# Optimization experiments

Measured on AMD Instinct MI355X. Metric: run time of the kernel, lower is better.

## Reference

```python
import jax, jax.numpy as jnp
import numpy as np

B, S, E, H = 8, 1024, 1152, 16  # batch, seq, embed_dim, num_heads
D = E // H  # head_dim = 72


def setup_inputs() -> dict:
    k = jax.random.key(0)
    ks = jax.random.split(k, 5)
    s_in = (2.0 / (E + E)) ** 0.5  # xavier-ish scale for packed proj
    return {
        "query": jax.random.normal(ks[0], (B, S, E), jnp.float32),
        "key": jax.random.normal(ks[1], (B, S, E), jnp.float32),
        "value": jax.random.normal(ks[2], (B, S, E), jnp.float32),
        "in_proj_weight": jax.random.normal(ks[3], (E, 3 * E), jnp.float32) * s_in,
        "in_proj_bias": jnp.zeros((3 * E,), jnp.float32),
        "out_w": jax.random.normal(ks[4], (E, E), jnp.float32) * s_in,
        "out_b": jnp.zeros((E,), jnp.float32),
    }


def reference(query, key, value, in_proj_weight, in_proj_bias, out_w, out_b):
    qb_, ss, _ = query.shape
    b, s, _ = value.shape
    qb, kb, vb = jnp.split(in_proj_bias, 3, -1)
    qw, kw, vw = jnp.split(in_proj_weight, 3, -1)
    q = (query @ qw + qb).reshape(qb_, ss, H, D)
    k = (key @ kw + kb).reshape(b, s, H, D)
    v = (value @ vw + vb).reshape(b, s, H, D)
    scale = D ** (-0.5)
    scores = jnp.einsum("bqhd,bkhd->bhqk", q * scale, k)  # [B,H,Sq,Sk]
    attn = jnp.einsum("bhqk,bkhd->bqhd", jax.nn.softmax(scores, axis=-1), v)
    return attn.reshape(qb_, ss, E) @ out_w + out_b
```

## Files before the change

kernel.cpp:

```cpp
#include <hip/hip_runtime.h>
#include <hip/hip_bf16.h>
#include <math.h>
#include <stdint.h>

static constexpr int Bb = 8, S = 1024, E = 1152, H = 16, D = 72;
static constexpr int N3 = 3 * E;
static constexpr long QKV_T = (long)Bb * H * S * D;

typedef __attribute__((ext_vector_type(8))) short bf16x8;
typedef __attribute__((ext_vector_type(4))) short bf16x4;
typedef __attribute__((ext_vector_type(4))) float f32x4;

#define MFMA16(A, B, C) __builtin_amdgcn_mfma_f32_16x16x32_bf16(A, B, C, 0, 0, 0)

__device__ __forceinline__ short f2bf(float f) {
    __hip_bfloat16 h = __float2bfloat16(f);
    return __builtin_bit_cast(short, h);
}
__device__ __forceinline__ unsigned packbf(float lo, float hi) {
    return (unsigned)(unsigned short)f2bf(lo) | ((unsigned)(unsigned short)f2bf(hi) << 16);
}

__device__ __forceinline__ void gload_lds16(const void* g, void* l) {
    __builtin_amdgcn_global_load_lds(
        (const __attribute__((address_space(1))) unsigned int*)g,
        (__attribute__((address_space(3))) unsigned int*)l, 16, 0, 0);
}

__global__ __launch_bounds__(256)
void wt_conv(const float* __restrict__ W, short* __restrict__ WT, int K, int N)
{
    __shared__ float tt[32][33];
    const int n0 = blockIdx.x * 32, k0 = blockIdx.y * 32;
    const int t = threadIdx.x;
    {
        int r = t >> 3, c4 = (t & 7) * 4;
        float4 v = *reinterpret_cast<const float4*>(W + (long)(k0 + r) * N + n0 + c4);
        tt[r][c4 + 0] = v.x; tt[r][c4 + 1] = v.y; tt[r][c4 + 2] = v.z; tt[r][c4 + 3] = v.w;
    }
    __syncthreads();
    {
        int n = t >> 3, k4 = (t & 7) * 4;
        bf16x4 o = {f2bf(tt[k4 + 0][n]), f2bf(tt[k4 + 1][n]),
                    f2bf(tt[k4 + 2][n]), f2bf(tt[k4 + 3][n])};
        *reinterpret_cast<bf16x4*>(WT + (long)(n0 + n) * K + k0 + k4) = o;
    }
}

__global__ __launch_bounds__(256)
void tobf16(const float* __restrict__ X, short* __restrict__ Y, long n4)
{
    for (long i = (long)blockIdx.x * 256 + threadIdx.x; i < n4; i += (long)gridDim.x * 256) {
        float4 v = reinterpret_cast<const float4*>(X)[i];
        bf16x4 o = {f2bf(v.x), f2bf(v.y), f2bf(v.z), f2bf(v.w)};
        reinterpret_cast<bf16x4*>(Y)[i] = o;
    }
}

__global__ __launch_bounds__(256)
void qkv_proj_one(const short* __restrict__ Xb, const short* __restrict__ WTn,
                  const float* __restrict__ bias, short* __restrict__ qkvW, int which)
{
    __shared__ short aT[128][32], bW[128][32];
    const int tid = threadIdx.x, lane = tid & 63, w = tid >> 6;
    const int c = lane & 15, g = lane >> 4;
    const int m0 = blockIdx.x * 128, n0 = blockIdx.y * 128;
    const int wm = (w >> 1) * 64, wn = (w & 1) * 64;
    const int lrow = lane >> 2, lch = (lane & 3) * 8;

    f32x4 acc[4][4] = {};

    for (int k0 = 0; k0 < E; k0 += 32) {
        __syncthreads();
        for (int t = 0; t < 2; ++t) {
            int row = w * 32 + t * 16;
            gload_lds16(Xb + (long)(m0 + row + lrow) * E + k0 + lch, &aT[row][0]);
            gload_lds16(WTn + (long)(n0 + row + lrow) * E + k0 + lch, &bW[row][0]);
        }
        __syncthreads();

        bf16x8 af[4], bh[4];
        for (int i = 0; i < 4; ++i) {
            af[i] = *reinterpret_cast<const bf16x8*>(&aT[wm + i * 16 + c][g * 8]);
            bh[i] = *reinterpret_cast<const bf16x8*>(&bW[wn + i * 16 + c][g * 8]);
        }
        for (int i = 0; i < 4; ++i)
            for (int j = 0; j < 4; ++j)
                acc[i][j] = MFMA16(af[i], bh[j], acc[i][j]);
    }

    for (int j = 0; j < 4; ++j) {
        int n = n0 + wn + j * 16 + c;
        float bv = bias[n];
        int hh = n / D, dd = n % D;
        if (which < 2) {
            for (int i = 0; i < 4; ++i) {
                int rowb = m0 + wm + i * 16 + g * 4;
                for (int r = 0; r < 4; ++r) {
                    int row = rowb + r;
                    int b = row >> 10, s = row & 1023;
                    qkvW[((long)(b * H + hh) * S + s) * D + dd] = f2bf(acc[i][j][r] + bv);
                }
            }
        } else {
            int cx = dd & 7;
            for (int i = 0; i < 4; ++i) {
                int srow = m0 + wm + i * 16 + g * 4;
                int b = srow >> 10, s = srow & 1023;
                int sw = (s & ~63) | ((((s >> 3) & 7) ^ cx) << 3) | (s & 7);
                bf16x4 pk = {f2bf(acc[i][j][0] + bv), f2bf(acc[i][j][1] + bv),
                             f2bf(acc[i][j][2] + bv), f2bf(acc[i][j][3] + bv)};
                *reinterpret_cast<bf16x4*>(&qkvW[((long)(b * H + hh) * D + dd) * S + sw]) = pk;
            }
        }
    }
}

__global__ __launch_bounds__(512, 4)
void attn_fwd(const short* __restrict__ qkv, short* __restrict__ attn)
{
    __shared__ short smem[28184];
    unsigned* PT = reinterpret_cast<unsigned*>(smem + 9752);
    const int tid = threadIdx.x, lane = tid & 63, w = tid >> 6;
    const int c = lane & 15, g = lane >> 4;
    const int bh = blockIdx.x;
    const int q0 = blockIdx.y * 256;
    const int b = bh >> 4, h = bh & 15;

    const short* Qb = qkv + (long)bh * (S * D);
    const short* Kb = qkv + QKV_T + (long)bh * (S * D);
    const short* Vt = qkv + 2 * QKV_T + (long)bh * ((long)D * S);

    if (tid < 24) smem[4608 + tid] = 0;
    if (tid < 512) smem[9240 + tid] = 0;

    const short* kg[2]; const short* vg[2]; int ldsOff[2];
    #pragma unroll
    for (int rr = 0; rr < 2; ++rr) {
        int r = w + rr * 8;
        int id = r * 64 + lane;
        kg[rr] = Kb + id * 8;
        vg[rr] = Vt + (long)(id >> 3) * S + (id & 7) * 8;
        ldsOff[rr] = id * 8;
    }

    bf16x8 qf[2][3];
    const bf16x8 zf = {};
    for (int i = 0; i < 2; ++i) {
        const short* qr = Qb + (long)(q0 + w * 32 + i * 16 + c) * D;
        qf[i][0] = *reinterpret_cast<const bf16x8*>(qr + g * 8);
        qf[i][1] = *reinterpret_cast<const bf16x8*>(qr + 32 + g * 8);
        qf[i][2] = (g == 0) ? *reinterpret_cast<const bf16x8*>(qr + 64) : zf;
    }

    const float K2 = 0.17003594880664552f;
    const float TH = 8.0f / K2;
    float m_run[2] = {-1e30f, -1e30f}, l_run[2] = {0.f, 0.f};
    f32x4 accO[5][2] = {};

    for (int kt = 0; kt < 16; ++kt) {
        __syncthreads();
        #pragma unroll
        for (int rr = 0; rr < 2; ++rr) {
            if (w + rr * 8 < 9) {
                gload_lds16(kg[rr], &smem[ldsOff[rr]]);
                gload_lds16(vg[rr], &smem[4632 + ldsOff[rr]]);
                kg[rr] += 64 * D;
                vg[rr] += 64;
            }
        }
        __syncthreads();

        f32x4 sT[4][2] = {};
        for (int dc = 0; dc < 3; ++dc) {
            for (int j = 0; j < 4; ++j) {
                bf16x8 kf = *reinterpret_cast<const bf16x8*>(
                    &smem[(j * 16 + c) * 72 + dc * 32 + g * 8]);
                for (int i = 0; i < 2; ++i)
                    sT[j][i] = MFMA16(kf, qf[i][dc], sT[j][i]);
            }
        }

        for (int i = 0; i < 2; ++i) {
            float mx = -1e30f;
            for (int j = 0; j < 4; ++j)
                for (int r = 0; r < 4; ++r) mx = fmaxf(mx, sT[j][i][r]);
            mx = fmaxf(mx, __shfl_xor(mx, 16));
            mx = fmaxf(mx, __shfl_xor(mx, 32));
            if (__any(mx > m_run[i] + TH)) {
                float m_new = fmaxf(m_run[i], mx);
                float corr = exp2f((m_run[i] - m_new) * K2);
                m_run[i] = m_new;
                l_run[i] *= corr;
                for (int n = 0; n < 5; ++n)
                    for (int r = 0; r < 4; ++r) accO[n][i][r] *= corr;
            }
            float mh = m_run[i] * K2;
            float ps = 0.f;
            for (int j = 0; j < 4; ++j) {
                float p0 = exp2f(fmaf(sT[j][i][0], K2, -mh));
                float p1 = exp2f(fmaf(sT[j][i][1], K2, -mh));
                float p2 = exp2f(fmaf(sT[j][i][2], K2, -mh));
                float p3 = exp2f(fmaf(sT[j][i][3], K2, -mh));
                ps += (p0 + p1) + (p2 + p3);
                PT[((w * 2 + i) * 16 + c) * 36 + j * 8 + g * 2 + 0] = packbf(p0, p1);
                PT[((w * 2 + i) * 16 + c) * 36 + j * 8 + g * 2 + 1] = packbf(p2, p3);
            }
            ps += __shfl_xor(ps, 16);
            ps += __shfl_xor(ps, 32);
            l_run[i] += ps;
        }

        for (int ks = 0; ks < 2; ++ks) {
            bf16x8 pf[2];
            for (int i = 0; i < 2; ++i)
                pf[i] = *reinterpret_cast<const bf16x8*>(
                    &PT[((w * 2 + i) * 16 + c) * 36 + ks * 16 + g * 4]);
            for (int n = 0; n < 5; ++n) {
                bf16x8 vf = *reinterpret_cast<const bf16x8*>(
                    &smem[4632 + (n * 16 + c) * 64 + (((ks * 4 + g) ^ (c & 7))) * 8]);
                for (int i = 0; i < 2; ++i)
                    accO[n][i] = MFMA16(vf, pf[i], accO[n][i]);
            }
        }
    }

    __syncthreads();
    for (int i = 0; i < 2; ++i) {
        float inv = 1.f / l_run[i];
        int ql = w * 32 + i * 16 + c;
        for (int n = 0; n < 5; ++n) {
            int d0 = n * 16 + g * 4;
            if (d0 >= D) continue;
            bf16x4 pk = {f2bf(accO[n][i][0] * inv), f2bf(accO[n][i][1] * inv),
                         f2bf(accO[n][i][2] * inv), f2bf(accO[n][i][3] * inv)};
            *reinterpret_cast<bf16x4*>(&smem[ql * 72 + d0]) = pk;
        }
    }
    __syncthreads();
    {
        const long rowbase = (long)(b * S + q0) * E + h * D;
        for (int ch = tid; ch < 2304; ch += 512) {
            int row = ch / 9, off = (ch % 9) * 8;
            *reinterpret_cast<uint4*>(attn + rowbase + (long)row * E + off) =
                *reinterpret_cast<const uint4*>(&smem[row * 72 + off]);
        }
    }
}

__global__ __launch_bounds__(256)
void out_proj(const short* __restrict__ Aat, const short* __restrict__ WTo,
              const float* __restrict__ bias, float* __restrict__ out)
{
    __shared__ short aT[128][32], bT[128][32];
    const int tid = threadIdx.x, lane = tid & 63, w = tid >> 6;
    const int c = lane & 15, g = lane >> 4;
    const int m0 = blockIdx.x * 128, n0 = blockIdx.y * 128;
    const int wm = (w >> 1) * 64, wn = (w & 1) * 64;
    const int lrow = lane >> 2, lch = (lane & 3) * 8;

    f32x4 acc[4][4] = {};
    for (int k0 = 0; k0 < E; k0 += 32) {
        __syncthreads();
        for (int t = 0; t < 2; ++t) {
            int row = w * 32 + t * 16;
            gload_lds16(Aat + (long)(m0 + row + lrow) * E + k0 + lch, &aT[row][0]);
            gload_lds16(WTo + (long)(n0 + row + lrow) * E + k0 + lch, &bT[row][0]);
        }
        __syncthreads();

        bf16x8 af[4], bf[4];
        for (int i = 0; i < 4; ++i) {
            af[i] = *reinterpret_cast<const bf16x8*>(&aT[wm + i * 16 + c][g * 8]);
            bf[i] = *reinterpret_cast<const bf16x8*>(&bT[wn + i * 16 + c][g * 8]);
        }
        for (int i = 0; i < 4; ++i)
            for (int j = 0; j < 4; ++j)
                acc[i][j] = MFMA16(af[i], bf[j], acc[i][j]);
    }

    for (int j = 0; j < 4; ++j) {
        int n = n0 + wn + j * 16 + c;
        float bv = bias[n];
        for (int i = 0; i < 4; ++i)
            for (int r = 0; r < 4; ++r) {
                int row = m0 + wm + i * 16 + g * 4 + r;
                out[(long)row * E + n] = acc[i][j][r] + bv;
            }
    }
}

extern "C" void kernel_launch(void* const* d_in, const int* in_sizes, int n_in,
                              void* d_out, int out_size, void* d_ws, size_t ws_size,
                              hipStream_t stream)
{
    const float* qin   = (const float*)d_in[0];
    const float* kin   = (const float*)d_in[1];
    const float* vin   = (const float*)d_in[2];
    const float* w_in  = (const float*)d_in[3];
    const float* b_in  = (const float*)d_in[4];
    const float* w_out = (const float*)d_in[5];
    const float* b_out = (const float*)d_in[6];

    short* ws  = (short*)d_ws;
    short* Q   = ws;
    short* K   = ws + QKV_T;
    short* V   = ws + 2 * QKV_T;
    short* A   = ws + 3 * QKV_T;
    short* WT  = ws + 4 * QKV_T;
    short* WTo = WT;
    float* out = (float*)d_out;

    wt_conv<<<dim3(108, 36), 256, 0, stream>>>(w_in, WT, E, N3);

    tobf16<<<2048, 256, 0, stream>>>(vin, A, QKV_T / 4);
    qkv_proj_one<<<dim3(64, 9), 256, 0, stream>>>(A, WT + 2L * E * E, b_in + 2 * E, V, 2);
    tobf16<<<2048, 256, 0, stream>>>(kin, A, QKV_T / 4);
    qkv_proj_one<<<dim3(64, 9), 256, 0, stream>>>(A, WT + 1L * E * E, b_in + E, K, 1);
    tobf16<<<2048, 256, 0, stream>>>(qin, A, QKV_T / 4);
    qkv_proj_one<<<dim3(64, 9), 256, 0, stream>>>(A, WT, b_in, Q, 0);

    attn_fwd<<<dim3(128, 4), 512, 0, stream>>>(ws, A);
    wt_conv<<<dim3(36, 36), 256, 0, stream>>>(w_out, WTo, E, E);
    out_proj<<<dim3(64, 9), 256, 0, stream>>>(A, WTo, b_out, out);
}
```

Measured before the change: 251.7 us.

## Fuse fp32-to-bf16 input conversion into QKV projection GEMM loads

Removes the three standalone tobf16 kernels and has the QKV projection load fp32 activations directly, converting them to bf16 in registers with the packed v_cvt_pk_bf16_f32 instruction before storing to LDS. This drops a full write and re-read of each bf16 activation copy plus three launches. In exchange, the A-tile path now uses synchronous register loads instead of the async global_load_lds path, and each A element is re-read from fp32 global memory by all 9 N-blocks. The attention kernel's bf16 packing also switches to the hardware packed convert.

```diff
diff --git a/kernel.cpp b/kernel.cpp
--- a/kernel.cpp
+++ b/kernel.cpp
@@ -17,8 +17,10 @@
     __hip_bfloat16 h = __float2bfloat16(f);
     return __builtin_bit_cast(short, h);
 }
-__device__ __forceinline__ unsigned packbf(float lo, float hi) {
-    return (unsigned)(unsigned short)f2bf(lo) | ((unsigned)(unsigned short)f2bf(hi) << 16);
+__device__ __forceinline__ unsigned cvtpk(float lo, float hi) {
+    unsigned r;
+    asm("v_cvt_pk_bf16_f32 %0, %1, %2" : "=v"(r) : "v"(lo), "v"(hi));
+    return r;
 }
 
 __device__ __forceinline__ void gload_lds16(const void* g, void* l) {
@@ -48,17 +50,7 @@
 }
 
 __global__ __launch_bounds__(256)
-void tobf16(const float* __restrict__ X, short* __restrict__ Y, long n4)
-{
-    for (long i = (long)blockIdx.x * 256 + threadIdx.x; i < n4; i += (long)gridDim.x * 256) {
-        float4 v = reinterpret_cast<const float4*>(X)[i];
-        bf16x4 o = {f2bf(v.x), f2bf(v.y), f2bf(v.z), f2bf(v.w)};
-        reinterpret_cast<bf16x4*>(Y)[i] = o;
-    }
-}
-
-__global__ __launch_bounds__(256)
-void qkv_proj_one(const short* __restrict__ Xb, const short* __restrict__ WTn,
+void qkv_proj_one(const float* __restrict__ Xf, const short* __restrict__ WTn,
                   const float* __restrict__ bias, short* __restrict__ qkvW, int which)
 {
     __shared__ short aT[128][32], bW[128][32];
@@ -67,6 +59,7 @@
     const int m0 = blockIdx.x * 128, n0 = blockIdx.y * 128;
     const int wm = (w >> 1) * 64, wn = (w & 1) * 64;
     const int lrow = lane >> 2, lch = (lane & 3) * 8;
+    const int ar = tid >> 1, ac = (tid & 1) * 16;
 
     f32x4 acc[4][4] = {};
 
@@ -74,8 +67,20 @@
         __syncthreads();
         for (int t = 0; t < 2; ++t) {
             int row = w * 32 + t * 16;
-            gload_lds16(Xb + (long)(m0 + row + lrow) * E + k0 + lch, &aT[row][0]);
             gload_lds16(WTn + (long)(n0 + row + lrow) * E + k0 + lch, &bW[row][0]);
+        }
+        {
+            const float* src = Xf + (long)(m0 + ar) * E + k0 + ac;
+            float4 a0 = *reinterpret_cast<const float4*>(src);
+            float4 a1 = *reinterpret_cast<const float4*>(src + 4);
+            float4 a2 = *reinterpret_cast<const float4*>(src + 8);
+            float4 a3 = *reinterpret_cast<const float4*>(src + 12);
+            uint4 p0 = {cvtpk(a0.x, a0.y), cvtpk(a0.z, a0.w),
+                        cvtpk(a1.x, a1.y), cvtpk(a1.z, a1.w)};
+            uint4 p1 = {cvtpk(a2.x, a2.y), cvtpk(a2.z, a2.w),
+                        cvtpk(a3.x, a3.y), cvtpk(a3.z, a3.w)};
+            *reinterpret_cast<uint4*>(&aT[ar][ac]) = p0;
+            *reinterpret_cast<uint4*>(&aT[ar][ac + 8]) = p1;
         }
         __syncthreads();
 
@@ -203,8 +208,8 @@
                 float p2 = exp2f(fmaf(sT[j][i][2], K2, -mh));
                 float p3 = exp2f(fmaf(sT[j][i][3], K2, -mh));
                 ps += (p0 + p1) + (p2 + p3);
-                PT[((w * 2 + i) * 16 + c) * 36 + j * 8 + g * 2 + 0] = packbf(p0, p1);
-                PT[((w * 2 + i) * 16 + c) * 36 + j * 8 + g * 2 + 1] = packbf(p2, p3);
+                PT[((w * 2 + i) * 16 + c) * 36 + j * 8 + g * 2 + 0] = cvtpk(p0, p1);
+                PT[((w * 2 + i) * 16 + c) * 36 + j * 8 + g * 2 + 1] = cvtpk(p2, p3);
             }
             ps += __shfl_xor(ps, 16);
             ps += __shfl_xor(ps, 32);
@@ -232,9 +237,9 @@
         for (int n = 0; n < 5; ++n) {
             int d0 = n * 16 + g * 4;
             if (d0 >= D) continue;
-            bf16x4 pk = {f2bf(accO[n][i][0] * inv), f2bf(accO[n][i][1] * inv),
-                         f2bf(accO[n][i][2] * inv), f2bf(accO[n][i][3] * inv)};
-            *reinterpret_cast<bf16x4*>(&smem[ql * 72 + d0]) = pk;
+            uint2 pk = {cvtpk(accO[n][i][0] * inv, accO[n][i][1] * inv),
+                        cvtpk(accO[n][i][2] * inv, accO[n][i][3] * inv)};
+            *reinterpret_cast<uint2*>(&smem[ql * 72 + d0]) = pk;
         }
     }
     __syncthreads();
@@ -313,12 +318,9 @@
 
     wt_conv<<<dim3(108, 36), 256, 0, stream>>>(w_in, WT, E, N3);
 
-    tobf16<<<2048, 256, 0, stream>>>(vin, A, QKV_T / 4);
-    qkv_proj_one<<<dim3(64, 9), 256, 0, stream>>>(A, WT + 2L * E * E, b_in + 2 * E, V, 2);
-    tobf16<<<2048, 256, 0, stream>>>(kin, A, QKV_T / 4);
-    qkv_proj_one<<<dim3(64, 9), 256, 0, stream>>>(A, WT + 1L * E * E, b_in + E, K, 1);
-    tobf16<<<2048, 256, 0, stream>>>(qin, A, QKV_T / 4);
-    qkv_proj_one<<<dim3(64, 9), 256, 0, stream>>>(A, WT, b_in, Q, 0);
+    qkv_proj_one<<<dim3(64, 9), 256, 0, stream>>>(vin, WT + 2L * E * E, b_in + 2 * E, V, 2);
+    qkv_proj_one<<<dim3(64, 9), 256, 0, stream>>>(kin, WT + 1L * E * E, b_in + E, K, 1);
+    qkv_proj_one<<<dim3(64, 9), 256, 0, stream>>>(qin, WT, b_in, Q, 0);
 
     attn_fwd<<<dim3(128, 4), 512, 0, stream>>>(ws, A);
     wt_conv<<<dim3(36, 36), 256, 0, stream>>>(w_out, WTo, E, E);
```

Measured after the change: 271.7 us. 1.08x slower.
